# Optimization experiments

Measured on AMD Instinct MI355X. Metric: run time of the kernel, lower is better.

The kernel has to match this reference:

```python
import jax, jax.numpy as jnp
import numpy as np

EMBED_DIM = 1024
B, L = 4, 2048

def setup_inputs() -> dict:
    key = jax.random.key(0)
    ks = jax.random.split(key, 7)
    d = EMBED_DIM
    s = 1.0 / np.sqrt(d)
    return {
        "x": jax.random.normal(ks[0], (B, L, d), dtype=jnp.float32),
        "Wq": jax.random.uniform(ks[1], (d, d), jnp.float32, -s, s),
        "bq": jax.random.uniform(ks[2], (d,), jnp.float32, -s, s),
        "Wk": jax.random.uniform(ks[3], (d, d), jnp.float32, -s, s),
        "bk": jax.random.uniform(ks[4], (d,), jnp.float32, -s, s),
        "Wv": jax.random.uniform(ks[5], (d, d), jnp.float32, -s, s),
        "bv": jax.random.uniform(ks[6], (d,), jnp.float32, -s, s),
    }

def reference(x, Wq, bq, Wk, bk, Wv, bv):
    Bsz, Lq, d = x.shape
    # torch Linear: x @ W.T + b
    Q = jnp.einsum("bld,ed->ble", x, Wq) + bq
    K = jnp.einsum("bld,ed->ble", x, Wk) + bk
    V = jnp.einsum("bld,ed->ble", x, Wv) + bv
    # additive causal mask: strict upper triangle gets -999 (NOT -inf), per source
    mask = jnp.triu(jnp.ones((Lq, Lq), dtype=x.dtype), k=1) * (-999.0)
    scores = jnp.einsum("bqd,bkd->bqk", Q, K) / jnp.asarray(d, x.dtype) ** 0.5 + mask
    wts = jax.nn.softmax(scores, axis=2)
    out = jnp.einsum("bqk,bkd->bqd", wts, V)
    return (out, wts)
```

## Files before the change

### kernel.cpp

```cpp
#include <hip/hip_runtime.h>
#include <hip/hip_bf16.h>
#include <stdint.h>

#define BATCH 4
#define L_SEQ 2048
#define DIM   1024

typedef __bf16 bf16;
typedef __bf16 bf16x4 __attribute__((ext_vector_type(4)));
typedef __bf16 bf16x8 __attribute__((ext_vector_type(8)));
typedef float  f32x4  __attribute__((ext_vector_type(4)));

#define GLDS(src, dst) __builtin_amdgcn_global_load_lds(\
    (const __attribute__((address_space(1))) void*)(src), \
    (__attribute__((address_space(3))) void*)(dst), 16, 0, 0)

#define BARX() do { asm volatile("" ::: "memory"); \
                    __builtin_amdgcn_s_barrier(); \
                    asm volatile("" ::: "memory"); } while (0)

#define MFMA16 __builtin_amdgcn_mfma_f32_16x16x32_bf16

__global__ __launch_bounds__(256)
void cvt_all(const float* __restrict__ x,  const float* __restrict__ Wq,
             const float* __restrict__ Wk, const float* __restrict__ Wv,
             bf16* __restrict__ Xb, bf16* __restrict__ Wcat)
{
    const int b = blockIdx.x;
    const float* src; bf16* dst; int i;
    if (b < 8192) { src = x; dst = Xb; i = b * 256 + threadIdx.x; }
    else {
        int s = (b - 8192) >> 10;
        src = s == 0 ? Wq : (s == 1 ? Wk : Wv);
        dst = Wcat + (size_t)s * 1048576;
        i = ((b - 8192) & 1023) * 256 + threadIdx.x;
    }
    float4 v = ((const float4*)src)[i];
    bf16x4 o = { (bf16)v.x, (bf16)v.y, (bf16)v.z, (bf16)v.w };
    ((bf16x4*)dst)[i] = o;
}

template<int MODE>
__global__ __launch_bounds__(256, 2)
void gemmQ(const bf16* __restrict__ Abase, const bf16* __restrict__ Bbase,
           const float* __restrict__ bqp, const float* __restrict__ bkp,
           const float* __restrict__ bvp,
           void* __restrict__ o0, void* __restrict__ o1, void* __restrict__ o2)
{
    constexpr int PST = 32768;
    __shared__ __align__(16) char smem[65536];

    int m0, n0, nt, z = blockIdx.z;
    const bf16 *Aop, *Bop;
    int lda, ldb;

    if constexpr (MODE == 0) {
        const int id = blockIdx.x, xcd = id & 7, r = id >> 3;
        const int mi = r >> 3;
        const int ni = xcd * 8 + (r & 7);
        m0 = mi * 128; n0 = ni * 128; nt = 16;
        Aop = Abase; Bop = Bbase; lda = DIM; ldb = DIM;
    } else if constexpr (MODE == 2) {
        const int u = blockIdx.x;
        const int qi = u >> 4, ki = u & 15;
        if (ki > qi) {
            float* sc = (float*)o0 + (size_t)z * L_SEQ * L_SEQ;
            const int row = qi * 128 + (threadIdx.x >> 1);
            float* p = sc + (size_t)row * L_SEQ + ki * 128 + (threadIdx.x & 1) * 64;
            f32x4 z4 = {0.f, 0.f, 0.f, 0.f};
#pragma unroll
            for (int c = 0; c < 16; ++c) *(f32x4*)(p + c * 4) = z4;
            return;
        }
        m0 = ki * 128; n0 = qi * 128; nt = 16;
        Aop = Abase + (size_t)z * L_SEQ * DIM;
        Bop = Bbase + (size_t)z * L_SEQ * DIM;
        lda = DIM; ldb = DIM;
    } else {
        const int id = blockIdx.x, k = id >> 1;
        const int qi = (id & 1) ? (k >> 5) : 15 - (k >> 5);
        const int rem = k & 31, ei = rem >> 2;
        z = rem & 3;
        m0 = ei * 128; n0 = qi * 128; nt = 2 * qi + 2;
        Aop = Abase + (size_t)z * DIM * L_SEQ;
        Bop = Bbase + (size_t)z * L_SEQ * L_SEQ;
        lda = L_SEQ; ldb = L_SEQ;
    }

    const int tid  = threadIdx.x;
    const int w    = tid >> 6, lane = tid & 63;
    const int wm   = w >> 1, wn = w & 1;
    const int l15  = lane & 15, lh = lane >> 4;
    const int lr4  = lh << 2;

    auto stageA = [&](int t) {
#pragma unroll
        for (int s = 0; s < 4; ++s) {
            const int p = s * 4096 + tid * 16;
            const int L = p ^ (((p >> 7) & 7) << 4);
            GLDS(Aop + (size_t)(m0 + (p >> 7)) * lda + ((t << 6) + ((L & 127) >> 1)),
                 smem + (t & 1) * PST + (p - (lane << 4)));
        }
    };
    auto stageB = [&](int t) {
#pragma unroll
        for (int s = 0; s < 4; ++s) {
            const int p = s * 4096 + tid * 16;
            const int L = p ^ (((p >> 7) & 7) << 4);
            GLDS(Bop + (size_t)(n0 + (p >> 7)) * ldb + ((t << 6) + ((L & 127) >> 1)),
                 smem + (t & 1) * PST + 16384 + (p - (lane << 4)));
        }
    };

    const int swz = (l15 & 7) << 4;
    const int ko0 = (lh << 4) ^ swz;
    const int ko1 = (64 + (lh << 4)) ^ swz;
    const int aro = (wm * 64 + l15) * 128;
    const int bro = 16384 + (wn * 64 + l15) * 128;

    f32x4 acc[4][4];
#pragma unroll
    for (int i = 0; i < 4; ++i)
#pragma unroll
        for (int j = 0; j < 4; ++j) acc[i][j] = (f32x4){0.f, 0.f, 0.f, 0.f};

    stageA(0); stageB(0); stageA(1); stageB(1);
    asm volatile("s_waitcnt vmcnt(8)" ::: "memory");
    __builtin_amdgcn_s_barrier();
    asm volatile("" ::: "memory");

    auto ktile = [&](int t) {
        const bool pref = (t + 2 < nt);
        char* base = smem + (t & 1) * PST;
        bf16x8 af[2][2], bfr[4][2];

#pragma unroll
        for (int i = 0; i < 2; ++i) {
            int ro = aro + i * 2048;
            af[i][0] = *(const bf16x8*)(base + ro + ko0);
            af[i][1] = *(const bf16x8*)(base + ro + ko1);
        }
#pragma unroll
        for (int j = 0; j < 2; ++j) {
            int ro = bro + j * 2048;
            bfr[j][0] = *(const bf16x8*)(base + ro + ko0);
            bfr[j][1] = *(const bf16x8*)(base + ro + ko1);
        }
        BARX();
        __builtin_amdgcn_s_setprio(1);
#pragma unroll
        for (int i = 0; i < 2; ++i)
#pragma unroll
            for (int j = 0; j < 2; ++j) {
                acc[i][j] = MFMA16(af[i][0], bfr[j][0], acc[i][j], 0, 0, 0);
                acc[i][j] = MFMA16(af[i][1], bfr[j][1], acc[i][j], 0, 0, 0);
            }
        __builtin_amdgcn_s_setprio(0);
        BARX();

#pragma unroll
        for (int j = 0; j < 2; ++j) {
            int ro = bro + (j + 2) * 2048;
            bfr[j + 2][0] = *(const bf16x8*)(base + ro + ko0);
            bfr[j + 2][1] = *(const bf16x8*)(base + ro + ko1);
        }
        BARX();
        __builtin_amdgcn_s_setprio(1);
#pragma unroll
        for (int i = 0; i < 2; ++i)
#pragma unroll
            for (int j = 0; j < 2; ++j) {
                acc[i][j + 2] = MFMA16(af[i][0], bfr[j + 2][0], acc[i][j + 2], 0, 0, 0);
                acc[i][j + 2] = MFMA16(af[i][1], bfr[j + 2][1], acc[i][j + 2], 0, 0, 0);
            }
        __builtin_amdgcn_s_setprio(0);
        BARX();

#pragma unroll
        for (int i = 0; i < 2; ++i) {
            int ro = aro + (i + 2) * 2048;
            af[i][0] = *(const bf16x8*)(base + ro + ko0);
            af[i][1] = *(const bf16x8*)(base + ro + ko1);
        }
        if (pref) stageB(t + 2);
        BARX();
        __builtin_amdgcn_s_setprio(1);
#pragma unroll
        for (int i = 0; i < 2; ++i)
#pragma unroll
            for (int j = 0; j < 2; ++j) {
                acc[i + 2][j + 2] = MFMA16(af[i][0], bfr[j + 2][0], acc[i + 2][j + 2], 0, 0, 0);
                acc[i + 2][j + 2] = MFMA16(af[i][1], bfr[j + 2][1], acc[i + 2][j + 2], 0, 0, 0);
            }
        __builtin_amdgcn_s_setprio(0);
        BARX();

        if (pref) stageA(t + 2);
        BARX();
        __builtin_amdgcn_s_setprio(1);
#pragma unroll
        for (int i = 0; i < 2; ++i)
#pragma unroll
            for (int j = 0; j < 2; ++j) {
                acc[i + 2][j] = MFMA16(af[i][0], bfr[j][0], acc[i + 2][j], 0, 0, 0);
                acc[i + 2][j] = MFMA16(af[i][1], bfr[j][1], acc[i + 2][j], 0, 0, 0);
            }
        __builtin_amdgcn_s_setprio(0);
        if (pref)            asm volatile("s_waitcnt vmcnt(8)" ::: "memory");
        else if (t + 1 < nt) asm volatile("s_waitcnt vmcnt(0)" ::: "memory");
        BARX();
    };

    for (int t = 0; t < nt; t += 2) { ktile(t); ktile(t + 1); }

    if constexpr (MODE == 0) {
        const int sel = m0 >> 10;
        const int eb  = (m0 & 1023) + wm * 64;
        if (sel < 2) {
            bf16* out = sel == 0 ? (bf16*)o0 : (bf16*)o1;
            const float* bias = sel == 0 ? bqp : bkp;
#pragma unroll
            for (int i = 0; i < 4; ++i) {
                int e0 = eb + i * 16 + lr4;
                float4 bb = *(const float4*)(bias + e0);
#pragma unroll
                for (int j = 0; j < 4; ++j) {
                    int l = n0 + wn * 64 + j * 16 + l15;
                    bf16x4 v = { (bf16)(acc[i][j][0] + bb.x), (bf16)(acc[i][j][1] + bb.y),
                                 (bf16)(acc[i][j][2] + bb.z), (bf16)(acc[i][j][3] + bb.w) };
                    *(bf16x4*)((bf16*)out + (size_t)l * DIM + e0) = v;
                }
            }
        } else {
            bf16* Vt = (bf16*)o2;
#pragma unroll
            for (int i = 0; i < 4; ++i) {
                int e0 = eb + i * 16 + lr4;
                float4 bb = *(const float4*)(bvp + e0);
                float bbr[4] = { bb.x, bb.y, bb.z, bb.w };
#pragma unroll
                for (int j = 0; j < 4; ++j) {
                    int lg = n0 + wn * 64 + j * 16 + l15;
                    int b = lg >> 11, l = lg & 2047;
#pragma unroll
                    for (int r = 0; r < 4; ++r)
                        Vt[((size_t)b * DIM + e0 + r) * L_SEQ + l] = (bf16)(acc[i][j][r] + bbr[r]);
                }
            }
        }
    } else if constexpr (MODE == 2) {
        float* sc = (float*)o0 + (size_t)z * L_SEQ * L_SEQ;
#pragma unroll
        for (int i = 0; i < 4; ++i) {
            int k0e = m0 + wm * 64 + i * 16 + lr4;
#pragma unroll
            for (int j = 0; j < 4; ++j) {
                int q = n0 + wn * 64 + j * 16 + l15;
                f32x4 v = acc[i][j] * 0.03125f;
                *(f32x4*)(sc + (size_t)q * L_SEQ + k0e) = v;
            }
        }
    } else {
        float* o = (float*)o0 + (size_t)z * L_SEQ * DIM;
#pragma unroll
        for (int i = 0; i < 4; ++i) {
            int e0 = m0 + wm * 64 + i * 16 + lr4;
#pragma unroll
            for (int j = 0; j < 4; ++j) {
                int q = n0 + wn * 64 + j * 16 + l15;
                *(f32x4*)(o + (size_t)q * DIM + e0) = acc[i][j];
            }
        }
    }
}

__global__ __launch_bounds__(256)
void softmax_rows(float* __restrict__ wts, bf16* __restrict__ Pb)
{
    const int row = blockIdx.x;
    const int q = row & 2047;
    float* s = wts + (size_t)row * L_SEQ;
    bf16*  p = Pb  + (size_t)row * L_SEQ;
    const int t = threadIdx.x;
    const int lane = t & 63, w = t >> 6;
    const int k0 = t * 8;

    float v[8];
    if (k0 + 7 <= q) {
        float4 a = *(const float4*)(s + k0);
        float4 b = *(const float4*)(s + k0 + 4);
        v[0]=a.x; v[1]=a.y; v[2]=a.z; v[3]=a.w;
        v[4]=b.x; v[5]=b.y; v[6]=b.z; v[7]=b.w;
    } else {
#pragma unroll
        for (int c = 0; c < 8; ++c) {
            int k = k0 + c;
            v[c] = (k <= q) ? s[k] : -3.0e38f;
        }
    }

    float mx = v[0];
#pragma unroll
    for (int c = 1; c < 8; ++c) mx = fmaxf(mx, v[c]);
#pragma unroll
    for (int off = 32; off; off >>= 1) mx = fmaxf(mx, __shfl_xor(mx, off));
    __shared__ float redm[4];
    if (lane == 0) redm[w] = mx;
    __syncthreads();
    mx = fmaxf(fmaxf(redm[0], redm[1]), fmaxf(redm[2], redm[3]));

    float sm = 0.f;
#pragma unroll
    for (int c = 0; c < 8; ++c) {
        float e = __expf(v[c] - mx);
        v[c] = e;
        sm += e;
    }
#pragma unroll
    for (int off = 32; off; off >>= 1) sm += __shfl_xor(sm, off);
    __shared__ float reds[4];
    if (lane == 0) reds[w] = sm;
    __syncthreads();
    sm = reds[0] + reds[1] + reds[2] + reds[3];
    const float inv = 1.f / sm;

    if (k0 <= (q | 127)) {
        float o[8];
#pragma unroll
        for (int c = 0; c < 8; ++c) o[c] = v[c] * inv;
        float4 s0 = { o[0], o[1], o[2], o[3] };
        float4 s1 = { o[4], o[5], o[6], o[7] };
        *(float4*)(s + k0)     = s0;
        *(float4*)(s + k0 + 4) = s1;
        bf16x8 pb = { (bf16)o[0], (bf16)o[1], (bf16)o[2], (bf16)o[3],
                      (bf16)o[4], (bf16)o[5], (bf16)o[6], (bf16)o[7] };
        *(bf16x8*)(p + k0) = pb;
    }
}

extern "C" void kernel_launch(void* const* d_in, const int* in_sizes, int n_in,
                              void* d_out, int out_size, void* d_ws, size_t ws_size,
                              hipStream_t stream)
{
    const float* x  = (const float*)d_in[0];
    const float* Wq = (const float*)d_in[1];
    const float* bq = (const float*)d_in[2];
    const float* Wk = (const float*)d_in[3];
    const float* bk = (const float*)d_in[4];
    const float* Wv = (const float*)d_in[5];
    const float* bv = (const float*)d_in[6];

    float* out = (float*)d_out;
    float* wts = out + (size_t)BATCH * L_SEQ * DIM;

    char* ws = (char*)d_ws;
    bf16* Xb   = (bf16*)(ws + 0);
    bf16* Wcat = (bf16*)(ws + (16u  << 20));
    bf16* Qb   = (bf16*)(ws + (22u  << 20));
    bf16* Kb   = (bf16*)(ws + (38u  << 20));
    bf16* Vt   = (bf16*)(ws + (54u  << 20));
    bf16* Pb   = (bf16*)(ws + (70u  << 20));

    cvt_all<<<dim3(11264), dim3(256), 0, stream>>>(x, Wq, Wk, Wv, Xb, Wcat);

    gemmQ<0><<<dim3(1536, 1, 1), dim3(256), 0, stream>>>(
        Wcat, Xb, bq, bk, bv, Qb, Kb, Vt);
    gemmQ<2><<<dim3(256, 1, 4), dim3(256), 0, stream>>>(
        Kb, Qb, nullptr, nullptr, nullptr, wts, nullptr, nullptr);
    softmax_rows<<<dim3(8192), dim3(256), 0, stream>>>(wts, Pb);
    gemmQ<3><<<dim3(512, 1, 1), dim3(256), 0, stream>>>(
        Vt, Pb, nullptr, nullptr, nullptr, out, nullptr, nullptr);
}
```

Measured before the change: 167.3 us.

## Restructure QKV projection k-loop with single-barrier prefetch and remap PV block order

For the projection GEMM (MODE 0), the per-tile loop now loads all A and B fragments from LDS up front, waits, and passes one barrier. It then issues the next tile's global-to-LDS prefetch and runs all 32 MFMAs in one block, instead of the split two-half ktile schedule with several barriers. Separately, the PV kernel's block-index decode changes so that the first and second halves of the grid take ascending and descending query tiles, rather than interleaving them by odd/even id. The goal is fewer barriers and better overlap in the projection, plus a different load-balance ordering for the causal PV work. In exchange, more fragment registers are live at once, which could raise register pressure.

Result: faster. 162.9 us (-2.7%).

```diff
diff --git a/kernel.cpp b/kernel.cpp
--- a/kernel.cpp
+++ b/kernel.cpp
@@ -77,10 +77,12 @@
         Bop = Bbase + (size_t)z * L_SEQ * DIM;
         lda = DIM; ldb = DIM;
     } else {
-        const int id = blockIdx.x, k = id >> 1;
-        const int qi = (id & 1) ? (k >> 5) : 15 - (k >> 5);
-        const int rem = k & 31, ei = rem >> 2;
-        z = rem & 3;
+        const int id = blockIdx.x;
+        const int hi = id >> 8, lo = id & 255;
+        const int q3 = lo >> 5;
+        const int qi = hi ? (15 - q3) : q3;
+        const int ei = (lo >> 2) & 7;
+        z = lo & 3;
         m0 = ei * 128; n0 = qi * 128; nt = 2 * qi + 2;
         Aop = Abase + (size_t)z * DIM * L_SEQ;
         Bop = Bbase + (size_t)z * L_SEQ * L_SEQ;
@@ -211,7 +213,43 @@
         BARX();
     };
 
-    for (int t = 0; t < nt; t += 2) { ktile(t); ktile(t + 1); }
+    if constexpr (MODE == 0) {
+        for (int t = 0; t < nt; ++t) {
+            const bool pref = (t + 2 < nt);
+            char* base = smem + (t & 1) * PST;
+            bf16x8 af[4][2], bfr[4][2];
+#pragma unroll
+            for (int i = 0; i < 4; ++i) {
+                int ro = aro + i * 2048;
+                af[i][0] = *(const bf16x8*)(base + ro + ko0);
+                af[i][1] = *(const bf16x8*)(base + ro + ko1);
+            }
+#pragma unroll
+            for (int j = 0; j < 4; ++j) {
+                int ro = bro + j * 2048;
+                bfr[j][0] = *(const bf16x8*)(base + ro + ko0);
+                bfr[j][1] = *(const bf16x8*)(base + ro + ko1);
+            }
+            asm volatile("s_waitcnt lgkmcnt(0)" ::: "memory");
+            __builtin_amdgcn_s_barrier();
+            asm volatile("" ::: "memory");
+            if (pref) { stageB(t + 2); stageA(t + 2); }
+            __builtin_amdgcn_s_setprio(1);
+#pragma unroll
+            for (int i = 0; i < 4; ++i)
+#pragma unroll
+                for (int j = 0; j < 4; ++j) {
+                    acc[i][j] = MFMA16(af[i][0], bfr[j][0], acc[i][j], 0, 0, 0);
+                    acc[i][j] = MFMA16(af[i][1], bfr[j][1], acc[i][j], 0, 0, 0);
+                }
+            __builtin_amdgcn_s_setprio(0);
+            if (pref)            asm volatile("s_waitcnt vmcnt(8)" ::: "memory");
+            else if (t + 1 < nt) asm volatile("s_waitcnt vmcnt(0)" ::: "memory");
+            BARX();
+        }
+    } else {
+        for (int t = 0; t < nt; t += 2) { ktile(t); ktile(t + 1); }
+    }
 
     if constexpr (MODE == 0) {
         const int sel = m0 >> 10;
```

## Restructure GEMM k-loop to load full fragments once and issue prefetch early

Applied to the files above, without the earlier changes.

Replaces the four-phase k-tile body, which interleaved LDS fragment reads, barriers and quarter-sized MFMA groups, with a single phase. That phase reads all A and B fragments, waits on LDS, issues both global-to-LDS prefetches, then runs all 32 MFMAs back to back. This removes three barriers per k-tile and gives the prefetch a longer window to overlap with compute, at the cost of more fragment registers live at once. It also remaps block indices in the PV mode so the two halves of the grid take mirrored query tiles in separate contiguous ranges, which changes how the triangular work is balanced.

After: 161.9 us. 1.03x faster.

```diff
diff --git a/kernel.cpp b/kernel.cpp
--- a/kernel.cpp
+++ b/kernel.cpp
@@ -77,10 +77,12 @@
         Bop = Bbase + (size_t)z * L_SEQ * DIM;
         lda = DIM; ldb = DIM;
     } else {
-        const int id = blockIdx.x, k = id >> 1;
-        const int qi = (id & 1) ? (k >> 5) : 15 - (k >> 5);
-        const int rem = k & 31, ei = rem >> 2;
-        z = rem & 3;
+        const int id = blockIdx.x;
+        const int hi = id >> 8, lo = id & 255;
+        const int q3 = lo >> 5;
+        const int qi = hi ? (15 - q3) : q3;
+        const int ei = (lo >> 2) & 7;
+        z = lo & 3;
         m0 = ei * 128; n0 = qi * 128; nt = 2 * qi + 2;
         Aop = Abase + (size_t)z * DIM * L_SEQ;
         Bop = Bbase + (size_t)z * L_SEQ * L_SEQ;
@@ -129,89 +131,39 @@
     __builtin_amdgcn_s_barrier();
     asm volatile("" ::: "memory");
 
-    auto ktile = [&](int t) {
+    for (int t = 0; t < nt; ++t) {
         const bool pref = (t + 2 < nt);
         char* base = smem + (t & 1) * PST;
-        bf16x8 af[2][2], bfr[4][2];
-
-#pragma unroll
-        for (int i = 0; i < 2; ++i) {
+        bf16x8 af[4][2], bfr[4][2];
+#pragma unroll
+        for (int i = 0; i < 4; ++i) {
             int ro = aro + i * 2048;
             af[i][0] = *(const bf16x8*)(base + ro + ko0);
             af[i][1] = *(const bf16x8*)(base + ro + ko1);
         }
 #pragma unroll
-        for (int j = 0; j < 2; ++j) {
+        for (int j = 0; j < 4; ++j) {
             int ro = bro + j * 2048;
             bfr[j][0] = *(const bf16x8*)(base + ro + ko0);
             bfr[j][1] = *(const bf16x8*)(base + ro + ko1);
         }
-        BARX();
+        asm volatile("s_waitcnt lgkmcnt(0)" ::: "memory");
+        __builtin_amdgcn_s_barrier();
+        asm volatile("" ::: "memory");
+        if (pref) { stageB(t + 2); stageA(t + 2); }
         __builtin_amdgcn_s_setprio(1);
 #pragma unroll
-        for (int i = 0; i < 2; ++i)
-#pragma unroll
-            for (int j = 0; j < 2; ++j) {
+        for (int i = 0; i < 4; ++i)
+#pragma unroll
+            for (int j = 0; j < 4; ++j) {
                 acc[i][j] = MFMA16(af[i][0], bfr[j][0], acc[i][j], 0, 0, 0);
                 acc[i][j] = MFMA16(af[i][1], bfr[j][1], acc[i][j], 0, 0, 0);
-            }
-        __builtin_amdgcn_s_setprio(0);
-        BARX();
-
-#pragma unroll
-        for (int j = 0; j < 2; ++j) {
-            int ro = bro + (j + 2) * 2048;
-            bfr[j + 2][0] = *(const bf16x8*)(base + ro + ko0);
-            bfr[j + 2][1] = *(const bf16x8*)(base + ro + ko1);
-        }
-        BARX();
-        __builtin_amdgcn_s_setprio(1);
-#pragma unroll
-        for (int i = 0; i < 2; ++i)
-#pragma unroll
-            for (int j = 0; j < 2; ++j) {
-                acc[i][j + 2] = MFMA16(af[i][0], bfr[j + 2][0], acc[i][j + 2], 0, 0, 0);
-                acc[i][j + 2] = MFMA16(af[i][1], bfr[j + 2][1], acc[i][j + 2], 0, 0, 0);
-            }
-        __builtin_amdgcn_s_setprio(0);
-        BARX();
-
-#pragma unroll
-        for (int i = 0; i < 2; ++i) {
-            int ro = aro + (i + 2) * 2048;
-            af[i][0] = *(const bf16x8*)(base + ro + ko0);
-            af[i][1] = *(const bf16x8*)(base + ro + ko1);
-        }
-        if (pref) stageB(t + 2);
-        BARX();
-        __builtin_amdgcn_s_setprio(1);
-#pragma unroll
-        for (int i = 0; i < 2; ++i)
-#pragma unroll
-            for (int j = 0; j < 2; ++j) {
-                acc[i + 2][j + 2] = MFMA16(af[i][0], bfr[j + 2][0], acc[i + 2][j + 2], 0, 0, 0);
-                acc[i + 2][j + 2] = MFMA16(af[i][1], bfr[j + 2][1], acc[i + 2][j + 2], 0, 0, 0);
-            }
-        __builtin_amdgcn_s_setprio(0);
-        BARX();
-
-        if (pref) stageA(t + 2);
-        BARX();
-        __builtin_amdgcn_s_setprio(1);
-#pragma unroll
-        for (int i = 0; i < 2; ++i)
-#pragma unroll
-            for (int j = 0; j < 2; ++j) {
-                acc[i + 2][j] = MFMA16(af[i][0], bfr[j][0], acc[i + 2][j], 0, 0, 0);
-                acc[i + 2][j] = MFMA16(af[i][1], bfr[j][1], acc[i + 2][j], 0, 0, 0);
             }
         __builtin_amdgcn_s_setprio(0);
         if (pref)            asm volatile("s_waitcnt vmcnt(8)" ::: "memory");
         else if (t + 1 < nt) asm volatile("s_waitcnt vmcnt(0)" ::: "memory");
         BARX();
-    };
-
-    for (int t = 0; t < nt; t += 2) { ktile(t); ktile(t + 1); }
+    }
 
     if constexpr (MODE == 0) {
         const int sel = m0 >> 10;
```
